# Kernel tuning notes

Hardware: AMD Instinct MI355X
Metric: run time of the kernel (lower is better)

Reference implementation:

```python
import jax, jax.numpy as jnp
import numpy as np

DT = 1e-3  # integration step (coeffs[3])
B, T = 512, 8192


def setup_inputs() -> dict:
    key = jax.random.key(0)
    k1, k2, k3, k4 = jax.random.split(key, 4)
    xicovs = jax.random.normal(k1, (B, T, 2, 2), dtype=jnp.float32) * 0.1
    dy = jax.random.normal(k2, (B, T, 2), dtype=jnp.float32) * 0.1
    # learned 2x2 kernel (initializer='uniform' in keras -> small uniform)
    coeffs_A = jax.random.uniform(k3, (2, 2), minval=-0.05, maxval=0.05, dtype=jnp.float32)
    # fixed measurement matrix C (coeffs[0])
    C = jnp.array([[0.5, 0.1], [-0.1, 0.5]], dtype=jnp.float32)
    del k4
    return {"xicovs": xicovs, "dy": dy, "coeffs_A": coeffs_A, "C": C}


def reference(xicovs, dy, coeffs_A, C):
    # xicovs: [B,T,2,2], dy: [B,T,2], coeffs_A/C: [2,2]
    b = xicovs.shape[0]
    x0 = jnp.tile(jnp.array([[1.0, 0.0]], dtype=xicovs.dtype), (b, 1))  # initial_state
    xic_tm = jnp.transpose(xicovs, (1, 0, 2, 3))  # [T,B,2,2] time-major
    dy_tm = jnp.transpose(dy, (1, 0, 2))          # [T,B,2]

    def step(x, inp):
        xic, dyt = inp
        # A - xicov @ C, per batch element
        A_mx = coeffs_A - jnp.einsum('bij,jk->bik', xic, C)
        out = jnp.einsum('ij,bj->bi', C, x) * DT          # emitted output uses prev state
        dx = jnp.einsum('bij,bj->bi', A_mx, x) * DT + jnp.einsum('bij,bj->bi', xic, dyt)
        return x + dx, out

    _, outs = jax.lax.scan(step, x0, (xic_tm, dy_tm))  # outs: [T,B,2]
    return jnp.transpose(outs, (1, 0, 2))  # [B,T,2] (return_sequences=True)
```

## Files before the change

### kernel.cpp

```cpp
#include <hip/hip_runtime.h>

namespace {

constexpr float kDT = 1e-3f;
constexpr int kB = 512;
constexpr int kT = 8192;
constexpr int kThreads = 1024;
constexpr int kWaves = kThreads / 64;
constexpr int kPassSteps = 2 * kThreads;
constexpr int kPasses = kT / kPassSteps;

struct Xf { float a, b, c, d, p, q; };

__device__ __forceinline__ Xf comp(const Xf& e, const Xf& l) {
  Xf o;
  o.a = l.a * e.a + l.b * e.c;
  o.b = l.a * e.b + l.b * e.d;
  o.c = l.c * e.a + l.d * e.c;
  o.d = l.c * e.b + l.d * e.d;
  o.p = l.a * e.p + l.b * e.q + l.p;
  o.q = l.c * e.p + l.d * e.q + l.q;
  return o;
}

template <int Ctrl, int RowMask>
__device__ __forceinline__ float dpp1(float v, float old) {
  return __int_as_float(__builtin_amdgcn_update_dpp(
      __float_as_int(old), __float_as_int(v), Ctrl, RowMask, 0xf, false));
}

template <int Ctrl, int RowMask>
__device__ __forceinline__ Xf dpp_xf(const Xf& v) {
  Xf r;
  r.a = dpp1<Ctrl, RowMask>(v.a, 1.0f);
  r.b = dpp1<Ctrl, RowMask>(v.b, 0.0f);
  r.c = dpp1<Ctrl, RowMask>(v.c, 0.0f);
  r.d = dpp1<Ctrl, RowMask>(v.d, 1.0f);
  r.p = dpp1<Ctrl, RowMask>(v.p, 0.0f);
  r.q = dpp1<Ctrl, RowMask>(v.q, 0.0f);
  return r;
}

__device__ __forceinline__ Xf wave_incl_scan(Xf x) {
  x = comp(dpp_xf<0x111, 0xf>(x), x);
  x = comp(dpp_xf<0x112, 0xf>(x), x);
  x = comp(dpp_xf<0x114, 0xf>(x), x);
  x = comp(dpp_xf<0x118, 0xf>(x), x);
  x = comp(dpp_xf<0x142, 0xa>(x), x);
  x = comp(dpp_xf<0x143, 0xc>(x), x);
  return x;
}

__device__ __forceinline__ Xf readlane_xf(const Xf& v, int l) {
  Xf r;
  r.a = __int_as_float(__builtin_amdgcn_readlane(__float_as_int(v.a), l));
  r.b = __int_as_float(__builtin_amdgcn_readlane(__float_as_int(v.b), l));
  r.c = __int_as_float(__builtin_amdgcn_readlane(__float_as_int(v.c), l));
  r.d = __int_as_float(__builtin_amdgcn_readlane(__float_as_int(v.d), l));
  r.p = __int_as_float(__builtin_amdgcn_readlane(__float_as_int(v.p), l));
  r.q = __int_as_float(__builtin_amdgcn_readlane(__float_as_int(v.q), l));
  return r;
}

__device__ __forceinline__ Xf make_xf(const float4 xv, float d0, float d1,
                                      float A00, float A01, float A10, float A11,
                                      float C00, float C01, float C10, float C11) {
  Xf m;
  m.a = 1.0f + kDT * (A00 - (xv.x * C00 + xv.y * C10));
  m.b =        kDT * (A01 - (xv.x * C01 + xv.y * C11));
  m.c =        kDT * (A10 - (xv.z * C00 + xv.w * C10));
  m.d = 1.0f + kDT * (A11 - (xv.z * C01 + xv.w * C11));
  m.p = xv.x * d0 + xv.y * d1;
  m.q = xv.z * d0 + xv.w * d1;
  return m;
}

__global__ __launch_bounds__(kThreads) void k_fused(
    const float* __restrict__ xic, const float* __restrict__ dy,
    const float* __restrict__ Ap, const float* __restrict__ Cp,
    float* __restrict__ out) {
  __shared__ float sWT[2][kWaves][6];

  const int tid = threadIdx.x;
  const int lane = tid & 63;
  const int w = tid >> 6;
  const size_t rbase = (size_t)blockIdx.x * kT;
  const size_t rbase2 = (size_t)blockIdx.x * (kT / 2);

  const float4* X4 = reinterpret_cast<const float4*>(xic);
  const float4* D4 = reinterpret_cast<const float4*>(dy);
  float4* O4 = reinterpret_cast<float4*>(out);

  const float A00 = Ap[0], A01 = Ap[1], A10 = Ap[2], A11 = Ap[3];
  const float C00 = Cp[0], C01 = Cp[1], C10 = Cp[2], C11 = Cp[3];

  float4 xva[2], xvb[2], dva[2];

  {
    const size_t s = (size_t)2 * tid;
    xva[0] = X4[rbase + s];
    xvb[0] = X4[rbase + s + 1];
    dva[0] = D4[rbase2 + tid];
  }

  float x0 = 1.0f, x1 = 0.0f;

#pragma unroll
  for (int c = 0; c < kPasses; ++c) {
    const int buf = c & 1;
    if (c + 1 < kPasses) {
      const size_t s = (size_t)(c + 1) * kPassSteps + 2 * tid;
      xva[buf ^ 1] = X4[rbase + s];
      xvb[buf ^ 1] = X4[rbase + s + 1];
      dva[buf ^ 1] = D4[rbase2 + (size_t)(c + 1) * kThreads + tid];
    }

    const Xf s0 = make_xf(xva[buf], dva[buf].x, dva[buf].y,
                          A00, A01, A10, A11, C00, C01, C10, C11);
    const Xf s1 = make_xf(xvb[buf], dva[buf].z, dva[buf].w,
                          A00, A01, A10, A11, C00, C01, C10, C11);
    const Xf tot = comp(s0, s1);

    const Xf inc = wave_incl_scan(tot);

    if (lane == 63) {
      sWT[buf][w][0] = inc.a; sWT[buf][w][1] = inc.b; sWT[buf][w][2] = inc.c;
      sWT[buf][w][3] = inc.d; sWT[buf][w][4] = inc.p; sWT[buf][w][5] = inc.q;
    }
    __syncthreads();

    Xf v{1.f, 0.f, 0.f, 1.f, 0.f, 0.f};
    if (lane < kWaves) {
      v = Xf{sWT[buf][lane][0], sWT[buf][lane][1], sWT[buf][lane][2],
             sWT[buf][lane][3], sWT[buf][lane][4], sWT[buf][lane][5]};
    }
    v = comp(dpp_xf<0x111, 0xf>(v), v);
    v = comp(dpp_xf<0x112, 0xf>(v), v);
    v = comp(dpp_xf<0x114, 0xf>(v), v);
    v = comp(dpp_xf<0x118, 0xf>(v), v);

    const Xf TT = readlane_xf(v, kWaves - 1);
    Xf Ew{1.f, 0.f, 0.f, 1.f, 0.f, 0.f};
    if (w > 0) Ew = readlane_xf(v, w - 1);

    const Xf le = dpp_xf<0x138, 0xf>(inc);

    const Xf ex = comp(Ew, le);

    const float e0 = ex.a * x0 + ex.b * x1 + ex.p;
    const float e1 = ex.c * x0 + ex.d * x1 + ex.q;

    float4 o;
    o.x = kDT * (C00 * e0 + C01 * e1);
    o.y = kDT * (C10 * e0 + C11 * e1);
    const float t0 = s0.a * e0 + s0.b * e1 + s0.p;
    const float t1 = s0.c * e0 + s0.d * e1 + s0.q;
    o.z = kDT * (C00 * t0 + C01 * t1);
    o.w = kDT * (C10 * t0 + C11 * t1);
    O4[rbase2 + (size_t)c * kThreads + tid] = o;

    if (c + 1 < kPasses) {
      const float n0 = TT.a * x0 + TT.b * x1 + TT.p;
      const float n1 = TT.c * x0 + TT.d * x1 + TT.q;
      x0 = n0; x1 = n1;
    }
  }
}

}

extern "C" void kernel_launch(void* const* d_in, const int* in_sizes, int n_in,
                              void* d_out, int out_size, void* d_ws,
                              size_t ws_size, hipStream_t stream) {
  const float* xic = (const float*)d_in[0];
  const float* dy  = (const float*)d_in[1];
  const float* Ap  = (const float*)d_in[2];
  const float* Cp  = (const float*)d_in[3];
  float* out = (float*)d_out;

  k_fused<<<kB, kThreads, 0, stream>>>(xic, dy, Ap, Cp, out);
}
```

Before: 30.23 us.

## Process two passes per barrier with a combined 32-entry cross-wave scan

Restructures the four sequential passes into two groups, each scanning two 2048-step chunks per barrier, so the block synchronizes twice instead of four times. Wave totals for both chunks go into shared memory and are combined with one 32-lane DPP scan. Explicit double-buffered prefetch is replaced by issuing both chunks' loads up front within a group, and launch bounds add an occupancy hint. This raises register pressure and gives up cross-group load prefetch.

```diff
diff --git a/kernel.cpp b/kernel.cpp
--- a/kernel.cpp
+++ b/kernel.cpp
@@ -7,8 +7,6 @@
 constexpr int kT = 8192;
 constexpr int kThreads = 1024;
 constexpr int kWaves = kThreads / 64;
-constexpr int kPassSteps = 2 * kThreads;
-constexpr int kPasses = kT / kPassSteps;
 
 struct Xf { float a, b, c, d, p, q; };
 
@@ -48,6 +46,15 @@
   x = comp(dpp_xf<0x118, 0xf>(x), x);
   x = comp(dpp_xf<0x142, 0xa>(x), x);
   x = comp(dpp_xf<0x143, 0xc>(x), x);
+  return x;
+}
+
+__device__ __forceinline__ Xf scan32(Xf x) {
+  x = comp(dpp_xf<0x111, 0xf>(x), x);
+  x = comp(dpp_xf<0x112, 0xf>(x), x);
+  x = comp(dpp_xf<0x114, 0xf>(x), x);
+  x = comp(dpp_xf<0x118, 0xf>(x), x);
+  x = comp(dpp_xf<0x142, 0xa>(x), x);
   return x;
 }
 
@@ -75,11 +82,11 @@
   return m;
 }
 
-__global__ __launch_bounds__(kThreads) void k_fused(
+__global__ __launch_bounds__(kThreads, 8) void k_fused(
     const float* __restrict__ xic, const float* __restrict__ dy,
     const float* __restrict__ Ap, const float* __restrict__ Cp,
     float* __restrict__ out) {
-  __shared__ float sWT[2][kWaves][6];
+  __shared__ float sWT[2][2][kWaves][6];
 
   const int tid = threadIdx.x;
   const int lane = tid & 63;
@@ -94,72 +101,89 @@
   const float A00 = Ap[0], A01 = Ap[1], A10 = Ap[2], A11 = Ap[3];
   const float C00 = Cp[0], C01 = Cp[1], C10 = Cp[2], C11 = Cp[3];
 
-  float4 xva[2], xvb[2], dva[2];
-
-  {
-    const size_t s = (size_t)2 * tid;
-    xva[0] = X4[rbase + s];
-    xvb[0] = X4[rbase + s + 1];
-    dva[0] = D4[rbase2 + tid];
-  }
-
   float x0 = 1.0f, x1 = 0.0f;
 
 #pragma unroll
-  for (int c = 0; c < kPasses; ++c) {
-    const int buf = c & 1;
-    if (c + 1 < kPasses) {
-      const size_t s = (size_t)(c + 1) * kPassSteps + 2 * tid;
-      xva[buf ^ 1] = X4[rbase + s];
-      xvb[buf ^ 1] = X4[rbase + s + 1];
-      dva[buf ^ 1] = D4[rbase2 + (size_t)(c + 1) * kThreads + tid];
-    }
-
-    const Xf s0 = make_xf(xva[buf], dva[buf].x, dva[buf].y,
-                          A00, A01, A10, A11, C00, C01, C10, C11);
-    const Xf s1 = make_xf(xvb[buf], dva[buf].z, dva[buf].w,
-                          A00, A01, A10, A11, C00, C01, C10, C11);
-    const Xf tot = comp(s0, s1);
-
-    const Xf inc = wave_incl_scan(tot);
-
+  for (int g = 0; g < 2; ++g) {
+    const size_t xb0i = rbase + (size_t)(2 * g) * 2048 + 2 * tid;
+    const size_t db0i = rbase2 + (size_t)(2 * g) * 1024 + tid;
+    const float4 xa0 = X4[xb0i];
+    const float4 xb0 = X4[xb0i + 1];
+    const float4 dv0 = D4[db0i];
+
+    const Xf s0_0 = make_xf(xa0, dv0.x, dv0.y,
+                            A00, A01, A10, A11, C00, C01, C10, C11);
+    const Xf s1_0 = make_xf(xb0, dv0.z, dv0.w,
+                            A00, A01, A10, A11, C00, C01, C10, C11);
+
+    const size_t xb1i = rbase + (size_t)(2 * g + 1) * 2048 + 2 * tid;
+    const size_t db1i = rbase2 + (size_t)(2 * g + 1) * 1024 + tid;
+    const float4 xa1 = X4[xb1i];
+    const float4 xb1 = X4[xb1i + 1];
+    const float4 dv1 = D4[db1i];
+
+    const Xf inc0 = wave_incl_scan(comp(s0_0, s1_0));
+    const Xf le0 = dpp_xf<0x138, 0xf>(inc0);
     if (lane == 63) {
-      sWT[buf][w][0] = inc.a; sWT[buf][w][1] = inc.b; sWT[buf][w][2] = inc.c;
-      sWT[buf][w][3] = inc.d; sWT[buf][w][4] = inc.p; sWT[buf][w][5] = inc.q;
+      sWT[g][0][w][0] = inc0.a; sWT[g][0][w][1] = inc0.b;
+      sWT[g][0][w][2] = inc0.c; sWT[g][0][w][3] = inc0.d;
+      sWT[g][0][w][4] = inc0.p; sWT[g][0][w][5] = inc0.q;
+    }
+
+    const Xf s0_1 = make_xf(xa1, dv1.x, dv1.y,
+                            A00, A01, A10, A11, C00, C01, C10, C11);
+    const Xf s1_1 = make_xf(xb1, dv1.z, dv1.w,
+                            A00, A01, A10, A11, C00, C01, C10, C11);
+    const Xf inc1 = wave_incl_scan(comp(s0_1, s1_1));
+    const Xf le1 = dpp_xf<0x138, 0xf>(inc1);
+    if (lane == 63) {
+      sWT[g][1][w][0] = inc1.a; sWT[g][1][w][1] = inc1.b;
+      sWT[g][1][w][2] = inc1.c; sWT[g][1][w][3] = inc1.d;
+      sWT[g][1][w][4] = inc1.p; sWT[g][1][w][5] = inc1.q;
     }
     __syncthreads();
 
     Xf v{1.f, 0.f, 0.f, 1.f, 0.f, 0.f};
-    if (lane < kWaves) {
-      v = Xf{sWT[buf][lane][0], sWT[buf][lane][1], sWT[buf][lane][2],
-             sWT[buf][lane][3], sWT[buf][lane][4], sWT[buf][lane][5]};
-    }
-    v = comp(dpp_xf<0x111, 0xf>(v), v);
-    v = comp(dpp_xf<0x112, 0xf>(v), v);
-    v = comp(dpp_xf<0x114, 0xf>(v), v);
-    v = comp(dpp_xf<0x118, 0xf>(v), v);
-
-    const Xf TT = readlane_xf(v, kWaves - 1);
-    Xf Ew{1.f, 0.f, 0.f, 1.f, 0.f, 0.f};
-    if (w > 0) Ew = readlane_xf(v, w - 1);
-
-    const Xf le = dpp_xf<0x138, 0xf>(inc);
-
-    const Xf ex = comp(Ew, le);
-
-    const float e0 = ex.a * x0 + ex.b * x1 + ex.p;
-    const float e1 = ex.c * x0 + ex.d * x1 + ex.q;
-
-    float4 o;
-    o.x = kDT * (C00 * e0 + C01 * e1);
-    o.y = kDT * (C10 * e0 + C11 * e1);
-    const float t0 = s0.a * e0 + s0.b * e1 + s0.p;
-    const float t1 = s0.c * e0 + s0.d * e1 + s0.q;
-    o.z = kDT * (C00 * t0 + C01 * t1);
-    o.w = kDT * (C10 * t0 + C11 * t1);
-    O4[rbase2 + (size_t)c * kThreads + tid] = o;
-
-    if (c + 1 < kPasses) {
+    if (lane < 32) {
+      const int sp = lane >> 4, wl = lane & 15;
+      v = Xf{sWT[g][sp][wl][0], sWT[g][sp][wl][1], sWT[g][sp][wl][2],
+             sWT[g][sp][wl][3], sWT[g][sp][wl][4], sWT[g][sp][wl][5]};
+    }
+    v = scan32(v);
+    const Xf TT = readlane_xf(v, 31);
+
+    {
+      Xf Ew{1.f, 0.f, 0.f, 1.f, 0.f, 0.f};
+      if (w > 0) Ew = readlane_xf(v, w - 1);
+      const Xf ex = comp(Ew, le0);
+      float e0 = ex.a * x0 + ex.b * x1 + ex.p;
+      float e1 = ex.c * x0 + ex.d * x1 + ex.q;
+      float4 o;
+      o.x = kDT * (C00 * e0 + C01 * e1);
+      o.y = kDT * (C10 * e0 + C11 * e1);
+      const float n0 = s0_0.a * e0 + s0_0.b * e1 + s0_0.p;
+      const float n1 = s0_0.c * e0 + s0_0.d * e1 + s0_0.q;
+      o.z = kDT * (C00 * n0 + C01 * n1);
+      o.w = kDT * (C10 * n0 + C11 * n1);
+      O4[db0i] = o;
+    }
+
+    {
+      const Xf Ew = readlane_xf(v, 15 + w);
+      const Xf ex = comp(Ew, le1);
+      float e0 = ex.a * x0 + ex.b * x1 + ex.p;
+      float e1 = ex.c * x0 + ex.d * x1 + ex.q;
+      float4 o;
+      o.x = kDT * (C00 * e0 + C01 * e1);
+      o.y = kDT * (C10 * e0 + C11 * e1);
+      const float n0 = s0_1.a * e0 + s0_1.b * e1 + s0_1.p;
+      const float n1 = s0_1.c * e0 + s0_1.d * e1 + s0_1.q;
+      o.z = kDT * (C00 * n0 + C01 * n1);
+      o.w = kDT * (C10 * n0 + C11 * n1);
+      O4[db1i] = o;
+    }
+
+    if (g == 0) {
       const float n0 = TT.a * x0 + TT.b * x1 + TT.p;
       const float n1 = TT.c * x0 + TT.d * x1 + TT.q;
       x0 = n0; x1 = n1;
```

New measurement: 29.98 us. Within noise of the previous version (-0.8%).
